# Performance work log

Measured on AMD Instinct MI355X. Metric: run time of the kernel, lower is better.

## Reference

```python
import jax, jax.numpy as jnp
import numpy as np

B, T, D = 1, 2048, 2048
HQ, HKV = 32, 8
DKV = 512  # HKV * head_dim

def setup_inputs() -> dict:
    key = jax.random.key(0)
    ks = jax.random.split(key, 5)
    s = 0.02
    return {
        "x": jax.random.normal(ks[0], (B, T, D), jnp.float32),
        "q_proj": jax.random.normal(ks[1], (D, D), jnp.float32) * s,
        "k_proj": jax.random.normal(ks[2], (DKV, D), jnp.float32) * s,
        "v_proj": jax.random.normal(ks[3], (DKV, D), jnp.float32) * s,
        "o_proj": jax.random.normal(ks[4], (D, D), jnp.float32) * s,
    }

def reference(x, q_proj, k_proj, v_proj, o_proj):
    b, t, _ = x.shape
    h_q, h_kv = HQ, HKV
    q_out = x @ q_proj.T            # [b,t,D]
    k_out = x @ k_proj.T            # [b,t,DKV]
    v_out = x @ v_proj.T
    dh_q = q_out.shape[-1] // h_q   # 64
    dh_k = k_out.shape[-1] // h_kv  # 64
    q = q_out.reshape(b, t, h_q, dh_q).transpose(0, 2, 1, 3)   # [b,hq,t,dh]
    k = k_out.reshape(b, t, h_kv, dh_k).transpose(0, 2, 1, 3)  # [b,hkv,t,dh]
    v = v_out.reshape(b, t, h_kv, dh_k).transpose(0, 2, 1, 3)
    group = h_q // h_kv
    k = jnp.repeat(k, group, axis=1)  # [b,hq,t,dh]
    v = jnp.repeat(v, group, axis=1)
    attn_logits = jnp.einsum('bhqd,bhkd->bhqk', q, k) / jnp.sqrt(jnp.float32(dh_q))
    mask = jnp.tril(jnp.ones((t, t), dtype=bool))
    attn = jax.nn.softmax(jnp.where(mask, attn_logits, -1e10), axis=-1)
    ctx = jnp.einsum('bhqk,bhkd->bhqd', attn, v)
    ctx = ctx.transpose(0, 2, 1, 3).reshape(b, t, o_proj.shape[0])
    return ctx @ o_proj
```

## Files before the change

### kernel.cpp

```cpp
#include <hip/hip_runtime.h>
#include <stdint.h>

typedef __attribute__((ext_vector_type(8))) __bf16 bf16x8;
typedef __attribute__((ext_vector_type(4))) float f32x4;
typedef __attribute__((ext_vector_type(4))) unsigned short u16x4;

typedef __attribute__((address_space(1))) unsigned int as1_uint;
typedef __attribute__((address_space(3))) unsigned int as3_uint;

__device__ __forceinline__ unsigned short f2bf(float f) {
  unsigned int u = __float_as_uint(f);
  u += 0x7fffu + ((u >> 16) & 1u);
  return (unsigned short)(u >> 16);
}

__device__ __forceinline__ void gload_lds16(const void* g, void* l) {
  __builtin_amdgcn_global_load_lds((as1_uint*)(uintptr_t)g, (as3_uint*)(uintptr_t)l,
                                   16, 0, 0);
}

__global__ __launch_bounds__(256)
void cvt_fused(const float* __restrict__ x, const float* __restrict__ qp,
               const float* __restrict__ kp, const float* __restrict__ vp,
               const float* __restrict__ op,
               unsigned short* __restrict__ xb, unsigned short* __restrict__ qpb,
               unsigned short* __restrict__ kpb, unsigned short* __restrict__ vpb,
               unsigned short* __restrict__ opT) {
  __shared__ unsigned short t[64][72];
  const int b = blockIdx.x;
  if (b < 10240) {
    const float* in;
    unsigned short* out;
    int base;
    if (b < 4096)      { in = x;  out = xb;  base = b; }
    else if (b < 8192) { in = qp; out = qpb; base = b - 4096; }
    else if (b < 9216) { in = kp; out = kpb; base = b - 8192; }
    else               { in = vp; out = vpb; base = b - 9216; }
    const int i = base * 256 + threadIdx.x;
    float4 v = ((const float4*)in)[i];
    u16x4 o;
    o[0] = f2bf(v.x); o[1] = f2bf(v.y); o[2] = f2bf(v.z); o[3] = f2bf(v.w);
    ((u16x4*)out)[i] = o;
    return;
  }
  const int tb = b - 10240;
  const int tj = (tb & 31) * 64;
  const int ti = (tb >> 5) * 64;
  const int r  = threadIdx.x >> 4;
  const int c4 = (threadIdx.x & 15) * 4;
#pragma unroll
  for (int i = 0; i < 4; ++i) {
    int row = r + i * 16;
    float4 v = *(const float4*)&op[(size_t)(ti + row) * 2048 + tj + c4];
    t[row][c4]     = f2bf(v.x);
    t[row][c4 + 1] = f2bf(v.y);
    t[row][c4 + 2] = f2bf(v.z);
    t[row][c4 + 3] = f2bf(v.w);
  }
  __syncthreads();
#pragma unroll
  for (int i = 0; i < 4; ++i) {
    int orow = r + i * 16;
    u16x4 o;
    o[0] = t[c4][orow]; o[1] = t[c4 + 1][orow];
    o[2] = t[c4 + 2][orow]; o[3] = t[c4 + 3][orow];
    *(u16x4*)&opT[(size_t)(tj + orow) * 2048 + ti + c4] = o;
  }
}

template <int BN, bool OUT_BF16>
__device__ __forceinline__
void gemm_body(const unsigned short* __restrict__ A,
               const unsigned short* __restrict__ B,
               void* __restrict__ Cout, int N, int K, float alpha,
               int bx, int by, unsigned short* lA, unsigned short* lB) {
  constexpr int NF  = BN / 32;
  constexpr int ASZ = 64 * 64;
  constexpr int BSZ = BN * 64;
  const int tid  = threadIdx.x;
  const int lane = tid & 63;
  const int w    = tid >> 6;
  const int wr   = (w >> 1) * 32;
  const int wc   = (w & 1) * (BN / 2);
  const long brow = (long)by * 64;
  const long bcol = (long)bx * BN;
  const int lr = lane & 15;
  const int lq = lane >> 4;

  const int row0 = tid >> 3;
  const int lc0  = (tid & 7) ^ (row0 & 7);

  f32x4 acc[2][NF] = {};

  const unsigned short* gA = A + (brow + row0) * (long)K + lc0 * 8;
  const unsigned short* gB = B + (bcol + row0) * (long)K + lc0 * 8;

#define G_STAGE(buf, k0)                                                          \
  {                                                                               \
    gload_lds16(gA + (k0),           lA + (buf) * ASZ + tid * 8);                 \
    gload_lds16(gA + 32l * K + (k0), lA + (buf) * ASZ + 2048 + tid * 8);          \
    _Pragma("unroll")                                                             \
    for (int g = 0; g < NF; ++g)                                                  \
      gload_lds16(gB + g * 32l * K + (k0), lB + (buf) * BSZ + g * 2048 + tid * 8);\
  }

  G_STAGE(0, 0);
  __syncthreads();

  for (int k0 = 0; k0 < K; k0 += 64) {
    const int cur = (k0 >> 6) & 1;
    if (k0 + 64 < K) G_STAGE(cur ^ 1, k0 + 64);
#pragma unroll
    for (int kk = 0; kk < 2; ++kk) {
      const int j = kk * 4 + lq;
      const int ra0 = wr + lr, ra1 = wr + 16 + lr;
      bf16x8 a0 = *(const bf16x8*)&lA[cur * ASZ + ra0 * 64 + ((j ^ (ra0 & 7)) << 3)];
      bf16x8 a1 = *(const bf16x8*)&lA[cur * ASZ + ra1 * 64 + ((j ^ (ra1 & 7)) << 3)];
      bf16x8 b[NF];
#pragma unroll
      for (int n = 0; n < NF; ++n) {
        const int rb = wc + n * 16 + lr;
        b[n] = *(const bf16x8*)&lB[cur * BSZ + rb * 64 + ((j ^ (rb & 7)) << 3)];
      }
#pragma unroll
      for (int n = 0; n < NF; ++n) {
        acc[0][n] = __builtin_amdgcn_mfma_f32_16x16x32_bf16(a0, b[n], acc[0][n], 0, 0, 0);
        acc[1][n] = __builtin_amdgcn_mfma_f32_16x16x32_bf16(a1, b[n], acc[1][n], 0, 0, 0);
      }
    }
    __syncthreads();
  }
#undef G_STAGE

  const int orow = (int)brow + wr + lq * 4;
  const int ocol = (int)bcol + wc + lr;
#pragma unroll
  for (int m = 0; m < 2; ++m)
#pragma unroll
    for (int n = 0; n < NF; ++n)
#pragma unroll
      for (int r = 0; r < 4; ++r) {
        size_t row = (size_t)(orow + m * 16 + r);
        size_t col = (size_t)(ocol + n * 16);
        float v = acc[m][n][r] * alpha;
        if (OUT_BF16)
          ((unsigned short*)Cout)[row * N + col] = f2bf(v);
        else
          ((float*)Cout)[row * N + col] = v;
      }
}

template <int BN, bool OUT_BF16>
__global__ __launch_bounds__(256)
void gemm_nt(const unsigned short* __restrict__ A,
             const unsigned short* __restrict__ B,
             void* __restrict__ Cout, int N, int K, float alpha) {
  __shared__ unsigned short lA[2 * 64 * 64];
  __shared__ unsigned short lB[2 * BN * 64];
  const int flat  = (int)blockIdx.x + (int)gridDim.x * (int)blockIdx.y;
  const int total = (int)(gridDim.x * gridDim.y);
  const int cpx   = total >> 3;
  const int swz   = (flat & 7) * cpx + (flat >> 3);
  const int bx    = swz % (int)gridDim.x;
  const int by    = swz / (int)gridDim.x;
  gemm_body<BN, OUT_BF16>(A, B, Cout, N, K, alpha, bx, by, lA, lB);
}

__global__ __launch_bounds__(256)
void gemm_proj(const unsigned short* __restrict__ xb,
               const unsigned short* __restrict__ qpb,
               const unsigned short* __restrict__ kpb,
               const unsigned short* __restrict__ vpb,
               unsigned short* __restrict__ Qb, unsigned short* __restrict__ Kbf,
               unsigned short* __restrict__ Vtb) {
  __shared__ unsigned short lA[2 * 64 * 64];
  __shared__ unsigned short lB[2 * 128 * 64];
  const int raw = blockIdx.x;
  const int bid = (raw & 7) * 96 + (raw >> 3);
  const unsigned short *A, *B;
  unsigned short* C;
  int N, bx, by;
  float alpha;
  if (bid < 512) {
    A = xb;  B = qpb; C = Qb;  N = 2048; alpha = 0.125f * 1.44269504088896f;
    bx = bid & 15; by = bid >> 4;
  } else if (bid < 640) {
    int b = bid - 512;
    A = xb;  B = kpb; C = Kbf; N = 512;  alpha = 1.0f;
    bx = b & 3; by = b >> 2;
  } else {
    int b = bid - 640;
    A = vpb; B = xb;  C = Vtb; N = 2048; alpha = 1.0f;
    bx = b & 15; by = b >> 4;
  }
  gemm_body<128, true>(A, B, C, N, 2048, alpha, bx, by, lA, lB);
}

__global__ __launch_bounds__(256, 4)
void attn64(const unsigned short* __restrict__ Q,
            const unsigned short* __restrict__ Kb,
            const unsigned short* __restrict__ Vt,
            unsigned short* __restrict__ ctx) {
  constexpr int T = 2048, DQ = 2048, DKV = 512, DH = 64;
  const int h    = blockIdx.x;
  const int hkv  = h >> 2;
  const int ya   = blockIdx.y >> 3;
  const int yb   = blockIdx.y & 7;
  const int qi   = (ya == 0) ? yb : (ya == 1) ? 15 - yb : (ya == 2) ? 16 + yb : 31 - yb;
  const int tid  = threadIdx.x;
  const int lane = tid & 63;
  const int w    = tid >> 6;
  const int lr   = lane & 15;
  const int lq   = lane >> 4;
  const int lk   = lq * 8;
  const int sw   = lr & 7;

  __shared__ unsigned short lK[2][64 * 64];
  __shared__ unsigned short lV[2][64 * 64];
  __shared__ unsigned short P[4][16][64];

  const int row0 = tid >> 3;
  const int lc0  = (tid & 7) ^ (row0 & 7);

  bf16x8 ones_frag;
#pragma unroll
  for (int i = 0; i < 8; ++i) ones_frag[i] = (lr == 0) ? (__bf16)1.0f : (__bf16)0.0f;

#define STAGE_KV(bufidx, kv0)                                                        \
  {                                                                                  \
    gload_lds16(Kb + (size_t)((kv0) + row0) * DKV + hkv * DH + lc0 * 8,              \
                &lK[bufidx][tid * 8]);                                               \
    gload_lds16(Kb + (size_t)((kv0) + row0 + 32) * DKV + hkv * DH + lc0 * 8,         \
                &lK[bufidx][2048 + tid * 8]);                                        \
    gload_lds16(Vt + (size_t)(hkv * DH + row0) * T + (kv0) + lc0 * 8,                \
                &lV[bufidx][tid * 8]);                                               \
    gload_lds16(Vt + (size_t)(hkv * DH + row0 + 32) * T + (kv0) + lc0 * 8,           \
                &lV[bufidx][2048 + tid * 8]);                                        \
  }

  const int q0b = qi * 64;
  const int qw  = q0b + w * 16;

  bf16x8 qf0 = *(const bf16x8*)&Q[(size_t)(qw + lr) * DQ + h * DH + lk];
  bf16x8 qf1 = *(const bf16x8*)&Q[(size_t)(qw + lr) * DQ + h * DH + 32 + lk];

  f32x4 oacc[4] = {};
  f32x4 lacc = {};
  float mr[4];
#pragma unroll
  for (int r = 0; r < 4; ++r) mr[r] = -3.0e38f;

  const int nt = qi + 1;
  STAGE_KV(0, 0);
  __syncthreads();

  for (int t = 0; t < nt; ++t) {
    const int kv0 = t * 64;
    const int cur = t & 1;
    if (t + 1 < nt) STAGE_KV(cur ^ 1, kv0 + 64);

    f32x4 s[4];
    __builtin_amdgcn_s_setprio(1);
#pragma unroll
    for (int n = 0; n < 4; ++n) {
      const int krow = n * 16 + lr;
      bf16x8 kf0 = *(const bf16x8*)&lK[cur][krow * 64 + ((lq ^ sw) << 3)];
      bf16x8 kf1 = *(const bf16x8*)&lK[cur][krow * 64 + (((4 + lq) ^ sw) << 3)];
      f32x4 acc = {};
      acc = __builtin_amdgcn_mfma_f32_16x16x32_bf16(qf0, kf0, acc, 0, 0, 0);
      acc = __builtin_amdgcn_mfma_f32_16x16x32_bf16(qf1, kf1, acc, 0, 0, 0);
      s[n] = acc;
    }
    __builtin_amdgcn_s_setprio(0);

    if (t == qi) {
      const int qr0 = qw + (lq << 2);
#pragma unroll
      for (int n = 0; n < 4; ++n) {
        int kc = kv0 + n * 16 + lr;
#pragma unroll
        for (int r = 0; r < 4; ++r)
          if (kc > qr0 + r) s[n][r] = -3.0e38f;
      }
    }

    float lml[4];
#pragma unroll
    for (int r = 0; r < 4; ++r)
      lml[r] = fmaxf(fmaxf(s[0][r], s[1][r]), fmaxf(s[2][r], s[3][r]));
    const bool defer = __all((lml[0] <= mr[0] + 8.f) & (lml[1] <= mr[1] + 8.f) &
                             (lml[2] <= mr[2] + 8.f) & (lml[3] <= mr[3] + 8.f));
    if (!defer) {
#pragma unroll
      for (int r = 0; r < 4; ++r) {
        float ml = lml[r];
        ml = fmaxf(ml, __shfl_xor(ml, 1));
        ml = fmaxf(ml, __shfl_xor(ml, 2));
        ml = fmaxf(ml, __shfl_xor(ml, 4));
        ml = fmaxf(ml, __shfl_xor(ml, 8));
        float mnew = fmaxf(mr[r], ml);
        float sc   = __builtin_amdgcn_exp2f(mr[r] - mnew);
        mr[r] = mnew;
        lacc[r] *= sc;
        oacc[0][r] *= sc; oacc[1][r] *= sc;
        oacc[2][r] *= sc; oacc[3][r] *= sc;
      }
    }

#pragma unroll
    for (int n = 0; n < 4; ++n)
#pragma unroll
      for (int r = 0; r < 4; ++r)
        s[n][r] = __builtin_amdgcn_exp2f(s[n][r] - mr[r]);

#pragma unroll
    for (int n = 0; n < 4; ++n)
#pragma unroll
      for (int r = 0; r < 4; ++r) {
        const int prow = (lq << 2) + r;
        P[w][prow][(((2 * n + (lr >> 3)) ^ (prow & 7)) << 3) + (lr & 7)] =
            (unsigned short)(__float_as_uint(s[n][r]) >> 16);
      }
    asm volatile("s_waitcnt lgkmcnt(0)" ::: "memory");
    __builtin_amdgcn_sched_barrier(0);

    __builtin_amdgcn_s_setprio(1);
#pragma unroll
    for (int ks = 0; ks < 2; ++ks) {
      bf16x8 pf = *(const bf16x8*)&P[w][lr][((ks * 4 + lq) ^ sw) << 3];
      lacc = __builtin_amdgcn_mfma_f32_16x16x32_bf16(pf, ones_frag, lacc, 0, 0, 0);
#pragma unroll
      for (int n = 0; n < 4; ++n) {
        const int vrow = n * 16 + lr;
        bf16x8 vf = *(const bf16x8*)&lV[cur][vrow * 64 + (((ks * 4 + lq) ^ sw) << 3)];
        oacc[n] = __builtin_amdgcn_mfma_f32_16x16x32_bf16(pf, vf, oacc[n], 0, 0, 0);
      }
    }
    __builtin_amdgcn_s_setprio(0);

    __syncthreads();
  }

  float inv[4];
#pragma unroll
  for (int r = 0; r < 4; ++r) {
    float l = __shfl(lacc[r], lane & 48);
    inv[r] = 1.f / l;
  }
#pragma unroll
  for (int n = 0; n < 4; ++n)
#pragma unroll
    for (int r = 0; r < 4; ++r) {
      int qrow = qw + (lq << 2) + r;
      ctx[(size_t)qrow * DQ + h * DH + n * 16 + lr] = f2bf(oacc[n][r] * inv[r]);
    }
#undef STAGE_KV
}

extern "C" void kernel_launch(void* const* d_in, const int* in_sizes, int n_in,
                              void* d_out, int out_size, void* d_ws, size_t ws_size,
                              hipStream_t stream) {
  const float* x  = (const float*)d_in[0];
  const float* qp = (const float*)d_in[1];
  const float* kp = (const float*)d_in[2];
  const float* vp = (const float*)d_in[3];
  const float* op = (const float*)d_in[4];

  char* ws = (char*)d_ws;
  const size_t MB = 1024 * 1024;
  unsigned short* xb   = (unsigned short*)(ws + 0 * MB);
  unsigned short* qpb  = (unsigned short*)(ws + 8 * MB);
  unsigned short* kpb  = (unsigned short*)(ws + 16 * MB);
  unsigned short* vpb  = (unsigned short*)(ws + 18 * MB);
  unsigned short* opT  = (unsigned short*)(ws + 20 * MB);
  unsigned short* Qb   = (unsigned short*)(ws + 28 * MB);
  unsigned short* Kbf  = (unsigned short*)(ws + 36 * MB);
  unsigned short* Vtb  = (unsigned short*)(ws + 38 * MB);
  unsigned short* ctxb = (unsigned short*)(ws + 40 * MB);

  cvt_fused<<<11264, 256, 0, stream>>>(x, qp, kp, vp, op, xb, qpb, kpb, vpb, opT);

  gemm_proj<<<768, 256, 0, stream>>>(xb, qpb, kpb, vpb, Qb, Kbf, Vtb);

  attn64<<<dim3(32, 32), 256, 0, stream>>>(Qb, Kbf, Vtb, ctxb);

  gemm_nt<128, false><<<dim3(16, 32), 256, 0, stream>>>(ctxb, opT, d_out, 2048, 2048, 1.0f);
}
```

Measured before the change: 112.7 us.

## Compute transposed S in attention so P stays in registers, dropping LDS round-trip

After: 110.8 us (median of 2 runs). Within noise of the previous version (-1.7%).

```diff
diff --git a/kernel.cpp b/kernel.cpp
--- a/kernel.cpp
+++ b/kernel.cpp
@@ -2,6 +2,7 @@
 #include <stdint.h>
 
 typedef __attribute__((ext_vector_type(8))) __bf16 bf16x8;
+typedef __attribute__((ext_vector_type(8))) unsigned short u16x8;
 typedef __attribute__((ext_vector_type(4))) float f32x4;
 typedef __attribute__((ext_vector_type(4))) unsigned short u16x4;
 
@@ -209,7 +210,6 @@
   const int qi   = (ya == 0) ? yb : (ya == 1) ? 15 - yb : (ya == 2) ? 16 + yb : 31 - yb;
   const int tid  = threadIdx.x;
   const int lane = tid & 63;
-  const int w    = tid >> 6;
   const int lr   = lane & 15;
   const int lq   = lane >> 4;
   const int lk   = lq * 8;
@@ -217,20 +217,16 @@
 
   __shared__ unsigned short lK[2][64 * 64];
   __shared__ unsigned short lV[2][64 * 64];
-  __shared__ unsigned short P[4][16][64];
 
   const int row0 = tid >> 3;
   const int lc0  = (tid & 7) ^ (row0 & 7);
-
-  bf16x8 ones_frag;
-#pragma unroll
-  for (int i = 0; i < 8; ++i) ones_frag[i] = (lr == 0) ? (__bf16)1.0f : (__bf16)0.0f;
+  const int kperm = 8 * ((row0 >> 2) & 3) + 4 * ((row0 >> 4) & 1) + (row0 & 3);
 
 #define STAGE_KV(bufidx, kv0)                                                        \
   {                                                                                  \
-    gload_lds16(Kb + (size_t)((kv0) + row0) * DKV + hkv * DH + lc0 * 8,              \
+    gload_lds16(Kb + (size_t)((kv0) + kperm) * DKV + hkv * DH + lc0 * 8,             \
                 &lK[bufidx][tid * 8]);                                               \
-    gload_lds16(Kb + (size_t)((kv0) + row0 + 32) * DKV + hkv * DH + lc0 * 8,         \
+    gload_lds16(Kb + (size_t)((kv0) + kperm + 32) * DKV + hkv * DH + lc0 * 8,        \
                 &lK[bufidx][2048 + tid * 8]);                                        \
     gload_lds16(Vt + (size_t)(hkv * DH + row0) * T + (kv0) + lc0 * 8,                \
                 &lV[bufidx][tid * 8]);                                               \
@@ -239,16 +235,14 @@
   }
 
   const int q0b = qi * 64;
-  const int qw  = q0b + w * 16;
+  const int qw  = q0b + (tid >> 6) * 16;
 
   bf16x8 qf0 = *(const bf16x8*)&Q[(size_t)(qw + lr) * DQ + h * DH + lk];
   bf16x8 qf1 = *(const bf16x8*)&Q[(size_t)(qw + lr) * DQ + h * DH + 32 + lk];
 
   f32x4 oacc[4] = {};
-  f32x4 lacc = {};
-  float mr[4];
-#pragma unroll
-  for (int r = 0; r < 4; ++r) mr[r] = -3.0e38f;
+  float l  = 0.f;
+  float mr = -3.0e38f;
 
   const int nt = qi + 1;
   STAGE_KV(0, 0);
@@ -267,73 +261,74 @@
       bf16x8 kf0 = *(const bf16x8*)&lK[cur][krow * 64 + ((lq ^ sw) << 3)];
       bf16x8 kf1 = *(const bf16x8*)&lK[cur][krow * 64 + (((4 + lq) ^ sw) << 3)];
       f32x4 acc = {};
-      acc = __builtin_amdgcn_mfma_f32_16x16x32_bf16(qf0, kf0, acc, 0, 0, 0);
-      acc = __builtin_amdgcn_mfma_f32_16x16x32_bf16(qf1, kf1, acc, 0, 0, 0);
+      acc = __builtin_amdgcn_mfma_f32_16x16x32_bf16(kf0, qf0, acc, 0, 0, 0);
+      acc = __builtin_amdgcn_mfma_f32_16x16x32_bf16(kf1, qf1, acc, 0, 0, 0);
       s[n] = acc;
     }
     __builtin_amdgcn_s_setprio(0);
 
     if (t == qi) {
-      const int qr0 = qw + (lq << 2);
+      const int kb = kv0 + 8 * lq;
+      const int qg = qw + lr;
 #pragma unroll
       for (int n = 0; n < 4; ++n) {
-        int kc = kv0 + n * 16 + lr;
+        const int kn = kb + 32 * (n >> 1) + 4 * (n & 1);
 #pragma unroll
         for (int r = 0; r < 4; ++r)
-          if (kc > qr0 + r) s[n][r] = -3.0e38f;
-      }
-    }
-
-    float lml[4];
-#pragma unroll
-    for (int r = 0; r < 4; ++r)
-      lml[r] = fmaxf(fmaxf(s[0][r], s[1][r]), fmaxf(s[2][r], s[3][r]));
-    const bool defer = __all((lml[0] <= mr[0] + 8.f) & (lml[1] <= mr[1] + 8.f) &
-                             (lml[2] <= mr[2] + 8.f) & (lml[3] <= mr[3] + 8.f));
+          if (kn + r > qg) s[n][r] = -3.0e38f;
+      }
+    }
+
+    float lml = fmaxf(fmaxf(fmaxf(s[0][0], s[0][1]), fmaxf(s[0][2], s[0][3])),
+                      fmaxf(fmaxf(s[1][0], s[1][1]), fmaxf(s[1][2], s[1][3])));
+    lml = fmaxf(lml, fmaxf(fmaxf(s[2][0], s[2][1]), fmaxf(s[2][2], s[2][3])));
+    lml = fmaxf(lml, fmaxf(fmaxf(s[3][0], s[3][1]), fmaxf(s[3][2], s[3][3])));
+    const bool defer = __all(lml <= mr + 8.f);
     if (!defer) {
+      float rm = lml;
+      rm = fmaxf(rm, __shfl_xor(rm, 16));
+      rm = fmaxf(rm, __shfl_xor(rm, 32));
+      float mnew = fmaxf(mr, rm);
+      float sc   = __builtin_amdgcn_exp2f(mr - mnew);
+      mr = mnew;
+      l *= sc;
+      float sc4[4];
+#pragma unroll
+      for (int r = 0; r < 4; ++r) sc4[r] = __shfl(sc, (lq << 2) + r);
+#pragma unroll
+      for (int m = 0; m < 4; ++m)
+#pragma unroll
+        for (int r = 0; r < 4; ++r) oacc[m][r] *= sc4[r];
+    }
+
+    u16x8 pk0, pk1;
+    float ps = 0.f;
+#pragma unroll
+    for (int n = 0; n < 4; ++n)
 #pragma unroll
       for (int r = 0; r < 4; ++r) {
-        float ml = lml[r];
-        ml = fmaxf(ml, __shfl_xor(ml, 1));
-        ml = fmaxf(ml, __shfl_xor(ml, 2));
-        ml = fmaxf(ml, __shfl_xor(ml, 4));
-        ml = fmaxf(ml, __shfl_xor(ml, 8));
-        float mnew = fmaxf(mr[r], ml);
-        float sc   = __builtin_amdgcn_exp2f(mr[r] - mnew);
-        mr[r] = mnew;
-        lacc[r] *= sc;
-        oacc[0][r] *= sc; oacc[1][r] *= sc;
-        oacc[2][r] *= sc; oacc[3][r] *= sc;
-      }
-    }
-
-#pragma unroll
-    for (int n = 0; n < 4; ++n)
-#pragma unroll
-      for (int r = 0; r < 4; ++r)
-        s[n][r] = __builtin_amdgcn_exp2f(s[n][r] - mr[r]);
-
-#pragma unroll
-    for (int n = 0; n < 4; ++n)
-#pragma unroll
-      for (int r = 0; r < 4; ++r) {
-        const int prow = (lq << 2) + r;
-        P[w][prow][(((2 * n + (lr >> 3)) ^ (prow & 7)) << 3) + (lr & 7)] =
-            (unsigned short)(__float_as_uint(s[n][r]) >> 16);
-      }
-    asm volatile("s_waitcnt lgkmcnt(0)" ::: "memory");
-    __builtin_amdgcn_sched_barrier(0);
+        float p = __builtin_amdgcn_exp2f(s[n][r] - mr);
+        unsigned int u = __float_as_uint(p);
+        ps += __uint_as_float(u & 0xFFFF0000u);
+        const int j = ((n & 1) << 2) + r;
+        if (n < 2) pk0[j] = (unsigned short)(u >> 16);
+        else       pk1[j] = (unsigned short)(u >> 16);
+      }
+    ps += __shfl_xor(ps, 16);
+    ps += __shfl_xor(ps, 32);
+    l += ps;
+    bf16x8 pf0 = *(bf16x8*)&pk0;
+    bf16x8 pf1 = *(bf16x8*)&pk1;
 
     __builtin_amdgcn_s_setprio(1);
 #pragma unroll
     for (int ks = 0; ks < 2; ++ks) {
-      bf16x8 pf = *(const bf16x8*)&P[w][lr][((ks * 4 + lq) ^ sw) << 3];
-      lacc = __builtin_amdgcn_mfma_f32_16x16x32_bf16(pf, ones_frag, lacc, 0, 0, 0);
-#pragma unroll
-      for (int n = 0; n < 4; ++n) {
-        const int vrow = n * 16 + lr;
+      bf16x8 pf = ks ? pf1 : pf0;
+#pragma unroll
+      for (int m = 0; m < 4; ++m) {
+        const int vrow = m * 16 + lr;
         bf16x8 vf = *(const bf16x8*)&lV[cur][vrow * 64 + (((ks * 4 + lq) ^ sw) << 3)];
-        oacc[n] = __builtin_amdgcn_mfma_f32_16x16x32_bf16(pf, vf, oacc[n], 0, 0, 0);
+        oacc[m] = __builtin_amdgcn_mfma_f32_16x16x32_bf16(pf, vf, oacc[m], 0, 0, 0);
       }
     }
     __builtin_amdgcn_s_setprio(0);
@@ -343,16 +338,14 @@
 
   float inv[4];
 #pragma unroll
-  for (int r = 0; r < 4; ++r) {
-    float l = __shfl(lacc[r], lane & 48);
-    inv[r] = 1.f / l;
-  }
-#pragma unroll
-  for (int n = 0; n < 4; ++n)
+  for (int r = 0; r < 4; ++r)
+    inv[r] = 1.f / __shfl(l, (lq << 2) + r);
+#pragma unroll
+  for (int m = 0; m < 4; ++m)
 #pragma unroll
     for (int r = 0; r < 4; ++r) {
       int qrow = qw + (lq << 2) + r;
-      ctx[(size_t)qrow * DQ + h * DH + n * 16 + lr] = f2bf(oacc[n][r] * inv[r]);
+      ctx[(size_t)qrow * DQ + h * DH + m * 16 + lr] = f2bf(oacc[m][r] * inv[r]);
     }
 #undef STAGE_KV
 }
```
